# Kernel tuning notes

Measured on AMD Instinct MI355X. Metric: run time of the kernel, lower is better.

The kernel has to match this reference:

```python
import jax, jax.numpy as jnp
import numpy as np

T, N, E, F_IN, C = 8, 50000, 800000, 64, 64


def setup_inputs() -> dict:
    key = jax.random.key(0)
    ks = jax.random.split(key, 32)
    inp = {
        "x": jax.random.normal(ks[0], (T, N, F_IN), dtype=jnp.float32),
        "edge_index": jax.random.randint(ks[1], (2, E), 0, N, dtype=jnp.int32),
        "edge_weight": jax.random.uniform(ks[2], (E,), dtype=jnp.float32),
    }
    s = 0.05
    names = ["xz", "hz", "xr", "hr", "xh", "hh"]
    for i, nm in enumerate(names):
        cin = F_IN if nm[0] == "x" else C
        inp[f"W{nm}0"] = jax.random.normal(ks[3 + 3 * i], (cin, C), dtype=jnp.float32) * s
        inp[f"W{nm}1"] = jax.random.normal(ks[4 + 3 * i], (cin, C), dtype=jnp.float32) * s
        inp[f"b{nm}"] = jax.random.normal(ks[5 + 3 * i], (C,), dtype=jnp.float32) * s
    inp["W_lin"] = jax.random.normal(ks[30], (C, 1), dtype=jnp.float32) * s
    inp["b_lin"] = jax.random.normal(ks[31], (1,), dtype=jnp.float32) * s
    return inp


def reference(x, edge_index, edge_weight,
              Wxz0, Wxz1, bxz, Whz0, Whz1, bhz,
              Wxr0, Wxr1, bxr, Whr0, Whr1, bhr,
              Wxh0, Wxh1, bxh, Whh0, Whh1, bhh,
              W_lin, b_lin):
    src, dst = edge_index[0], edge_index[1]
    n = x.shape[1]
    # sym-normalized L_hat = -D^{-1/2} A D^{-1/2} (ChebConv, lambda_max=2)
    deg = jnp.zeros((n,), x.dtype).at[src].add(edge_weight)
    dinv = jnp.where(deg > 0, jax.lax.rsqrt(jnp.maximum(deg, 1e-12)), 0.0)
    nw = -edge_weight * dinv[src] * dinv[dst]  # (E,)

    def cheb(v, W0, W1, b):
        # K=2 Chebyshev: v @ W0 + (L_hat v) @ W1 + b ; v: (T, N, Cin)
        msgs = nw[None, :, None] * v[:, src, :]          # (T, E, Cin)
        tx1 = jnp.zeros_like(v).at[:, dst, :].add(msgs)  # scatter-add over nodes
        return v @ W0 + tx1 @ W1 + b

    H = jnp.zeros(x.shape[:2] + (Whz0.shape[0],), x.dtype)  # H=None -> zeros
    Z = jax.nn.sigmoid(cheb(x, Wxz0, Wxz1, bxz) + cheb(H, Whz0, Whz1, bhz))
    R = jax.nn.sigmoid(cheb(x, Wxr0, Wxr1, bxr) + cheb(H, Whr0, Whr1, bhr))
    Ht = jnp.tanh(cheb(x, Wxh0, Wxh1, bxh) + cheb(R * H, Whh0, Whh1, bhh))
    H = Z * H + (1.0 - Z) * Ht
    h = jax.nn.relu(H)
    return h @ W_lin + b_lin
```

## Files before the change

kernel.cpp:

```cpp
#include <hip/hip_runtime.h>

#define T_ 8
#define N_ 50000
#define E_ 800000
#define C_ 64
#define OVF_CAP 131072

typedef __attribute__((ext_vector_type(8))) short bf16x8;
typedef __attribute__((ext_vector_type(4))) float f32x4;

__device__ inline short f2bf(float f) {
    union { float f; unsigned int u; } v; v.f = f;
    unsigned int u = v.u + 0x7FFFu + ((v.u >> 16) & 1u);
    return (short)(u >> 16);
}
__device__ inline float bf2f_lo(unsigned int u) {
    union { unsigned int u; float f; } v; v.u = u << 16;
    return v.f;
}
__device__ inline float bf2f_hi(unsigned int u) {
    union { unsigned int u; float f; } v; v.u = u & 0xffff0000u;
    return v.f;
}

__global__ __launch_bounds__(256) void fused_prep_kernel(
        const int* __restrict__ src, const int* __restrict__ dst,
        const float* __restrict__ w,
        float* __restrict__ degw, int* __restrict__ cnt,
        int2* __restrict__ es, int cap,
        int* __restrict__ ovfcnt, int4* __restrict__ ovf,
        const float* __restrict__ x, unsigned short* __restrict__ xb,
        const float* __restrict__ Wz0, const float* __restrict__ Wz1,
        const float* __restrict__ Wh0, const float* __restrict__ Wh1,
        short* __restrict__ swz) {
    if (blockIdx.x < 3125) {
        int e = blockIdx.x * 256 + threadIdx.x;
        int s = src[e], d = dst[e];
        float wv = w[e];
        atomicAdd(&degw[s], wv);
        int pos = atomicAdd(&cnt[d], 1);
        if (pos < cap) {
            es[d * cap + pos] = make_int2(s, __float_as_int(wv));
        } else {
            int op = atomicAdd(ovfcnt, 1);
            if (op < OVF_CAP) ovf[op] = make_int4(d, s, __float_as_int(wv), 0);
        }
    } else if (blockIdx.x < 15625) {
        int id = (blockIdx.x - 3125) * 256 + threadIdx.x;
        int c8 = id & 7;
        int t = (id >> 3) & 7;
        int n = id >> 6;
        const float* xr = x + ((long long)t * N_ + n) * C_ + c8 * 8;
        float4 a = *(const float4*)(xr);
        float4 b = *(const float4*)(xr + 4);
        bf16x8 o;
        o[0] = f2bf(a.x); o[1] = f2bf(a.y); o[2] = f2bf(a.z); o[3] = f2bf(a.w);
        o[4] = f2bf(b.x); o[5] = f2bf(b.y); o[6] = f2bf(b.z); o[7] = f2bf(b.w);
        *(bf16x8*)(xb + (long long)id * 8) = o;
    } else {
        int idx = (blockIdx.x - 15625) * 256 + threadIdx.x;
        int j = idx & 7;
        int lane = (idx >> 3) & 63;
        int kb = (idx >> 9) & 1;
        int c = (idx >> 10) & 3;
        int mat = idx >> 12;
        const float* W = (mat == 0) ? Wz0 : (mat == 1) ? Wz1 : (mat == 2) ? Wh0 : Wh1;
        int k = kb * 32 + (lane >> 4) * 8 + j;
        int n = c * 16 + (lane & 15);
        swz[idx] = f2bf(W[k * 64 + n]);
    }
}

#define ACC8(W, V)                                                       \
    acc[0] += (W) * bf2f_lo((V).x); acc[1] += (W) * bf2f_hi((V).x);      \
    acc[2] += (W) * bf2f_lo((V).y); acc[3] += (W) * bf2f_hi((V).y);      \
    acc[4] += (W) * bf2f_lo((V).z); acc[5] += (W) * bf2f_hi((V).z);      \
    acc[6] += (W) * bf2f_lo((V).w); acc[7] += (W) * bf2f_hi((V).w);

__global__ __launch_bounds__(256) void gather_node_kernel(
        const int* __restrict__ cnt, const int2* __restrict__ es, int cap,
        const float* __restrict__ degw,
        const int* __restrict__ ovfcnt, const int4* __restrict__ ovf,
        const unsigned short* __restrict__ xb, const short* __restrict__ swz,
        const float* __restrict__ bxz, const float* __restrict__ bhz,
        const float* __restrict__ bxh, const float* __restrict__ bhh,
        const float* __restrict__ Wlin, const float* __restrict__ blin,
        float* __restrict__ out) {
    __shared__ unsigned short ltx[32 * 72];
    __shared__ float laz[2][16][65];

    int lane = threadIdx.x & 63;
    int wid = threadIdx.x >> 6;
    int base = blockIdx.x * 4;

    {
        int d = base + wid;
        int t = lane >> 3;
        int oct = lane & 7;
        int m = cnt[d];
        int mb = m < cap ? m : cap;
        float dd = degw[d];
        float id = dd > 0.f ? rsqrtf(fmaxf(dd, 1e-12f)) : 0.f;

        int2 pk = (lane < mb) ? es[d * cap + lane] : make_int2(0, 0);
        float dsrc = degw[pk.x];
        float is = dsrc > 0.f ? rsqrtf(fmaxf(dsrc, 1e-12f)) : 0.f;
        float nw_l = -__int_as_float(pk.y) * is * id;

        float acc[8] = {0.f, 0.f, 0.f, 0.f, 0.f, 0.f, 0.f, 0.f};
        const unsigned short* xbase = xb + lane * 8;
        int k = 0;
        for (; k + 7 < mb; k += 8) {
            int ss[8]; float ww[8];
#pragma unroll
            for (int j = 0; j < 8; ++j) {
                ss[j] = __shfl(pk.x, k + j);
                ww[j] = __shfl(nw_l, k + j);
            }
            uint4 vv[8];
#pragma unroll
            for (int j = 0; j < 8; ++j)
                vv[j] = *(const uint4*)(xbase + (long long)ss[j] * 512);
#pragma unroll
            for (int j = 0; j < 8; ++j) { ACC8(ww[j], vv[j]); }
        }
        for (; k < mb; ++k) {
            int s0 = __shfl(pk.x, k);
            float w0 = __shfl(nw_l, k);
            uint4 v0 = *(const uint4*)(xbase + (long long)s0 * 512);
            ACC8(w0, v0);
        }
        if (m > cap) {
            int oc = *ovfcnt;
            if (oc > OVF_CAP) oc = OVF_CAP;
            for (int i = 0; i < oc; ++i) {
                int4 o = ovf[i];
                if (o.x == d) {
                    float ds = degw[o.y];
                    float is2 = ds > 0.f ? rsqrtf(fmaxf(ds, 1e-12f)) : 0.f;
                    float w0 = -__int_as_float(o.z) * is2 * id;
                    uint4 v0 = *(const uint4*)(xbase + (long long)o.y * 512);
                    ACC8(w0, v0);
                }
            }
        }
        uint4 ob;
        ob.x = (unsigned int)(unsigned short)f2bf(acc[0]) |
               ((unsigned int)(unsigned short)f2bf(acc[1]) << 16);
        ob.y = (unsigned int)(unsigned short)f2bf(acc[2]) |
               ((unsigned int)(unsigned short)f2bf(acc[3]) << 16);
        ob.z = (unsigned int)(unsigned short)f2bf(acc[4]) |
               ((unsigned int)(unsigned short)f2bf(acc[5]) << 16);
        ob.w = (unsigned int)(unsigned short)f2bf(acc[6]) |
               ((unsigned int)(unsigned short)f2bf(acc[7]) << 16);
        int r = wid * 8 + t;
        *(uint4*)(ltx + r * 72 + oct * 8) = ob;
    }
    __syncthreads();

    int mt = wid >> 1;
    int g = wid & 1;
    int c16 = lane & 15;
    int kq = lane >> 4;
    int r_blk = mt * 16 + c16;
    const unsigned short* xr = xb + (long long)(base * 8 + r_blk) * C_ + kq * 8;
    bf16x8 ax0 = *(const bf16x8*)(xr);
    bf16x8 ax1 = *(const bf16x8*)(xr + 32);
    bf16x8 at0 = *(const bf16x8*)(ltx + r_blk * 72 + kq * 8);
    bf16x8 at1 = *(const bf16x8*)(ltx + r_blk * 72 + 32 + kq * 8);

    const float* bA = g ? bxh : bxz;
    const float* bB = g ? bhh : bhz;
    const short* wA = swz + (2 * g) * 4096 + lane * 8;
    const short* wB = swz + (2 * g + 1) * 4096 + lane * 8;

    f32x4 a4[4];
#pragma unroll
    for (int c = 0; c < 4; ++c) {
        int col = c * 16 + c16;
        float bv = bA[col] + bB[col];
        a4[c] = (f32x4){bv, bv, bv, bv};
    }
#pragma unroll
    for (int c = 0; c < 4; ++c) {
        bf16x8 bA0 = *(const bf16x8*)(wA + (c * 2 + 0) * 512);
        bf16x8 bA1 = *(const bf16x8*)(wA + (c * 2 + 1) * 512);
        bf16x8 bB0 = *(const bf16x8*)(wB + (c * 2 + 0) * 512);
        bf16x8 bB1 = *(const bf16x8*)(wB + (c * 2 + 1) * 512);
        a4[c] = __builtin_amdgcn_mfma_f32_16x16x32_bf16(ax0, bA0, a4[c], 0, 0, 0);
        a4[c] = __builtin_amdgcn_mfma_f32_16x16x32_bf16(ax1, bA1, a4[c], 0, 0, 0);
        a4[c] = __builtin_amdgcn_mfma_f32_16x16x32_bf16(at0, bB0, a4[c], 0, 0, 0);
        a4[c] = __builtin_amdgcn_mfma_f32_16x16x32_bf16(at1, bB1, a4[c], 0, 0, 0);
    }

    if (g == 0) {
#pragma unroll
        for (int c = 0; c < 4; ++c)
#pragma unroll
            for (int r = 0; r < 4; ++r)
                laz[mt][kq * 4 + r][c * 16 + c16] = a4[c][r];
    }
    __syncthreads();
    if (g == 1) {
        float part[4] = {0.f, 0.f, 0.f, 0.f};
#pragma unroll
        for (int c = 0; c < 4; ++c) {
            int col = c * 16 + c16;
            float wl = Wlin[col];
#pragma unroll
            for (int r = 0; r < 4; ++r) {
                float a = laz[mt][kq * 4 + r][col];
                float b = a4[c][r];
                float z = 1.f / (1.f + __expf(-a));
                float aa = fabsf(b);
                float e = __expf(-2.f * aa);
                float ht = copysignf((1.f - e) / (1.f + e), b);
                float h = fmaxf((1.f - z) * ht, 0.f);
                part[r] += h * wl;
            }
        }
#pragma unroll
        for (int m = 1; m <= 8; m <<= 1) {
#pragma unroll
            for (int r = 0; r < 4; ++r) part[r] += __shfl_xor(part[r], m);
        }
        if (c16 == 0) {
            float bl = blin[0];
#pragma unroll
            for (int r = 0; r < 4; ++r) {
                int rb = mt * 16 + kq * 4 + r;
                out[(long long)(rb & 7) * N_ + base + (rb >> 3)] = part[r] + bl;
            }
        }
    }
}

extern "C" void kernel_launch(void* const* d_in, const int* in_sizes, int n_in,
                              void* d_out, int out_size, void* d_ws, size_t ws_size,
                              hipStream_t stream) {
    const float* x    = (const float*)d_in[0];
    const int*   ei   = (const int*)d_in[1];
    const float* w    = (const float*)d_in[2];
    const float* Wxz0 = (const float*)d_in[3];
    const float* Wxz1 = (const float*)d_in[4];
    const float* bxz  = (const float*)d_in[5];
    const float* bhz  = (const float*)d_in[8];
    const float* Wxh0 = (const float*)d_in[15];
    const float* Wxh1 = (const float*)d_in[16];
    const float* bxh  = (const float*)d_in[17];
    const float* bhh  = (const float*)d_in[20];
    const float* Wlin = (const float*)d_in[21];
    const float* blin = (const float*)d_in[22];
    float* out = (float*)d_out;

    const int* src = ei;
    const int* dst = ei + E_;

    char* ws = (char*)d_ws;
    size_t off = 0;
    auto alloc = [&](size_t bytes) {
        char* p = ws + off;
        off = (off + bytes + 511) & ~(size_t)511;
        return p;
    };
    short* swz         = (short*)alloc(4 * 4096 * sizeof(short));
    float* degw        = (float*)alloc((size_t)N_ * 4);
    int*   cnt         = (int*)alloc((size_t)N_ * 4);
    int*   ovfcnt      = (int*)alloc(512);
    int4*  ovf         = (int4*)alloc((size_t)OVF_CAP * 16);
    unsigned short* xb = (unsigned short*)alloc((size_t)T_ * N_ * C_ * 2);
    size_t fixed = off;

    int cap = 16;
    for (int c : {64, 48, 32, 24}) {
        if (fixed + (size_t)N_ * c * 8 + 512 <= ws_size) { cap = c; break; }
    }
    int2* es = (int2*)alloc((size_t)N_ * cap * 8);

    hipMemsetAsync(degw, 0, (size_t)N_ * 4, stream);
    hipMemsetAsync(cnt, 0, (size_t)N_ * 4, stream);
    hipMemsetAsync(ovfcnt, 0, 4, stream);

    fused_prep_kernel<<<15689, 256, 0, stream>>>(src, dst, w, degw, cnt,
                                                 es, cap, ovfcnt, ovf,
                                                 x, xb, Wxz0, Wxz1, Wxh0, Wxh1, swz);

    gather_node_kernel<<<N_ / 4, 256, 0, stream>>>(
        cnt, es, cap, degw, ovfcnt, ovf, xb, swz,
        bxz, bhz, bxh, bhh, Wlin, blin, out);
}
```

Baseline: 408.0 us.

## Precompute normalized edge weights in prep via separate degree histogram kernel

Result: no change. 407.5 us (-0.1%).

```diff
diff --git a/kernel.cpp b/kernel.cpp
--- a/kernel.cpp
+++ b/kernel.cpp
@@ -23,10 +23,17 @@
     return v.f;
 }
 
+__global__ __launch_bounds__(256) void hist_kernel(const int* __restrict__ src,
+                                                   const float* __restrict__ w,
+                                                   float* __restrict__ degw) {
+    int e = blockIdx.x * 256 + threadIdx.x;
+    atomicAdd(&degw[src[e]], w[e]);
+}
+
 __global__ __launch_bounds__(256) void fused_prep_kernel(
         const int* __restrict__ src, const int* __restrict__ dst,
-        const float* __restrict__ w,
-        float* __restrict__ degw, int* __restrict__ cnt,
+        const float* __restrict__ w, const float* __restrict__ degw,
+        int* __restrict__ cnt,
         int2* __restrict__ es, int cap,
         int* __restrict__ ovfcnt, int4* __restrict__ ovf,
         const float* __restrict__ x, unsigned short* __restrict__ xb,
@@ -36,14 +43,16 @@
     if (blockIdx.x < 3125) {
         int e = blockIdx.x * 256 + threadIdx.x;
         int s = src[e], d = dst[e];
-        float wv = w[e];
-        atomicAdd(&degw[s], wv);
+        float ds = degw[s], dd = degw[d];
+        float is = ds > 0.f ? rsqrtf(fmaxf(ds, 1e-12f)) : 0.f;
+        float idv = dd > 0.f ? rsqrtf(fmaxf(dd, 1e-12f)) : 0.f;
+        float nwv = -w[e] * is * idv;
         int pos = atomicAdd(&cnt[d], 1);
         if (pos < cap) {
-            es[d * cap + pos] = make_int2(s, __float_as_int(wv));
+            es[d * cap + pos] = make_int2(s, __float_as_int(nwv));
         } else {
             int op = atomicAdd(ovfcnt, 1);
-            if (op < OVF_CAP) ovf[op] = make_int4(d, s, __float_as_int(wv), 0);
+            if (op < OVF_CAP) ovf[op] = make_int4(d, s, __float_as_int(nwv), 0);
         }
     } else if (blockIdx.x < 15625) {
         int id = (blockIdx.x - 3125) * 256 + threadIdx.x;
@@ -79,7 +88,6 @@
 
 __global__ __launch_bounds__(256) void gather_node_kernel(
         const int* __restrict__ cnt, const int2* __restrict__ es, int cap,
-        const float* __restrict__ degw,
         const int* __restrict__ ovfcnt, const int4* __restrict__ ovf,
         const unsigned short* __restrict__ xb, const short* __restrict__ swz,
         const float* __restrict__ bxz, const float* __restrict__ bhz,
@@ -97,36 +105,34 @@
         int d = base + wid;
         int t = lane >> 3;
         int oct = lane & 7;
+        int2 pk = (lane < cap) ? es[d * cap + lane] : make_int2(0, 0);
         int m = cnt[d];
         int mb = m < cap ? m : cap;
-        float dd = degw[d];
-        float id = dd > 0.f ? rsqrtf(fmaxf(dd, 1e-12f)) : 0.f;
-
-        int2 pk = (lane < mb) ? es[d * cap + lane] : make_int2(0, 0);
-        float dsrc = degw[pk.x];
-        float is = dsrc > 0.f ? rsqrtf(fmaxf(dsrc, 1e-12f)) : 0.f;
-        float nw_l = -__int_as_float(pk.y) * is * id;
 
         float acc[8] = {0.f, 0.f, 0.f, 0.f, 0.f, 0.f, 0.f, 0.f};
         const unsigned short* xbase = xb + lane * 8;
         int k = 0;
-        for (; k + 7 < mb; k += 8) {
-            int ss[8]; float ww[8];
-#pragma unroll
-            for (int j = 0; j < 8; ++j) {
-                ss[j] = __shfl(pk.x, k + j);
-                ww[j] = __shfl(nw_l, k + j);
-            }
-            uint4 vv[8];
-#pragma unroll
-            for (int j = 0; j < 8; ++j)
-                vv[j] = *(const uint4*)(xbase + (long long)ss[j] * 512);
-#pragma unroll
-            for (int j = 0; j < 8; ++j) { ACC8(ww[j], vv[j]); }
+        for (; k + 3 < mb; k += 4) {
+            int s0 = __shfl(pk.x, k);
+            int s1 = __shfl(pk.x, k + 1);
+            int s2 = __shfl(pk.x, k + 2);
+            int s3 = __shfl(pk.x, k + 3);
+            uint4 v0 = *(const uint4*)(xbase + (long long)s0 * 512);
+            uint4 v1 = *(const uint4*)(xbase + (long long)s1 * 512);
+            uint4 v2 = *(const uint4*)(xbase + (long long)s2 * 512);
+            uint4 v3 = *(const uint4*)(xbase + (long long)s3 * 512);
+            float w0 = __int_as_float(__shfl(pk.y, k));
+            float w1 = __int_as_float(__shfl(pk.y, k + 1));
+            float w2 = __int_as_float(__shfl(pk.y, k + 2));
+            float w3 = __int_as_float(__shfl(pk.y, k + 3));
+            ACC8(w0, v0);
+            ACC8(w1, v1);
+            ACC8(w2, v2);
+            ACC8(w3, v3);
         }
         for (; k < mb; ++k) {
             int s0 = __shfl(pk.x, k);
-            float w0 = __shfl(nw_l, k);
+            float w0 = __int_as_float(__shfl(pk.y, k));
             uint4 v0 = *(const uint4*)(xbase + (long long)s0 * 512);
             ACC8(w0, v0);
         }
@@ -136,9 +142,7 @@
             for (int i = 0; i < oc; ++i) {
                 int4 o = ovf[i];
                 if (o.x == d) {
-                    float ds = degw[o.y];
-                    float is2 = ds > 0.f ? rsqrtf(fmaxf(ds, 1e-12f)) : 0.f;
-                    float w0 = -__int_as_float(o.z) * is2 * id;
+                    float w0 = __int_as_float(o.z);
                     uint4 v0 = *(const uint4*)(xbase + (long long)o.y * 512);
                     ACC8(w0, v0);
                 }
@@ -281,11 +285,13 @@
     hipMemsetAsync(cnt, 0, (size_t)N_ * 4, stream);
     hipMemsetAsync(ovfcnt, 0, 4, stream);
 
+    hist_kernel<<<3125, 256, 0, stream>>>(src, w, degw);
+
     fused_prep_kernel<<<15689, 256, 0, stream>>>(src, dst, w, degw, cnt,
                                                  es, cap, ovfcnt, ovf,
                                                  x, xb, Wxz0, Wxz1, Wxh0, Wxh1, swz);
 
     gather_node_kernel<<<N_ / 4, 256, 0, stream>>>(
-        cnt, es, cap, degw, ovfcnt, ovf, xb, swz,
+        cnt, es, cap, ovfcnt, ovf, xb, swz,
         bxz, bhz, bxh, bhh, Wlin, blin, out);
 }
```
